# Performance work log

Hardware: AMD Instinct MI355X
Metric: run time of the kernel (lower is better)

Reference implementation:

```python
import jax, jax.numpy as jnp
import numpy as np

H = 128      # hidden_dim
N = 200000   # number of available (job, machine) ops
M = 1000     # machine nodes
J = 5000     # job nodes


def setup_inputs() -> dict:
    key = jax.random.key(0)
    ks = jax.random.split(key, 8)
    s = 0.05  # weight scale
    return {
        "x_graph": jax.random.normal(ks[0], (1, 2 * H), jnp.float32),
        "x_m": jax.random.normal(ks[1], (M, H), jnp.float32),
        "x_job": jax.random.normal(ks[2], (J, H), jnp.float32),
        "m_ids": jax.random.randint(ks[3], (N,), 0, M),
        "job_idx": jax.random.randint(ks[4], (N,), 0, J),
        "W0": jax.random.normal(ks[5], (4 * H, H), jnp.float32) * s,
        "b0": jnp.zeros((H,), jnp.float32),
        "W1": jax.random.normal(ks[6], (H, H), jnp.float32) * s,
        "b1": jnp.zeros((H,), jnp.float32),
        "W2": jax.random.normal(ks[7], (H, 1), jnp.float32) * s,
        "b2": jnp.zeros((1,), jnp.float32),
    }


def reference(x_graph, x_m, x_job, m_ids, job_idx, W0, b0, W1, b1, W2, b2):
    n = m_ids.shape[0]
    # vectorized form of the python loop: [x_graph | x_m[m_id] | x_job[job_pos]] -> [N, 4H]
    feats = jnp.concatenate(
        [
            jnp.broadcast_to(x_graph, (n, x_graph.shape[1])),
            x_m[m_ids],
            x_job[job_idx],
        ],
        axis=1,
    )
    h = jax.nn.relu(feats @ W0 + b0)   # Linear(4H -> H) + ReLU
    h = jax.nn.relu(h @ W1 + b1)       # Linear(H -> H) + ReLU
    scores = (h @ W2 + b2)[:, 0]       # Linear(H -> 1), squeeze -> [N]
    logp = jax.nn.log_softmax(scores, axis=0)
    probs = jnp.exp(logp)
    idx = jnp.argmax(scores)           # greedy selection (deterministic baseline)
    entropy = -jnp.sum(probs * logp)   # Categorical entropy
    return idx, probs[idx], logp[idx], entropy
```

## Files before the change

kernel.cpp:

```cpp
#include <hip/hip_runtime.h>
#include <math.h>

#define HID 128
#define TILE_R 64
#define TILE_P 32
#define XS_STRIDE 132
#define H0S_STRIDE 136
#define DELTA 0.05f
#define MAIN_GRID 1042

typedef short bf16x8 __attribute__((ext_vector_type(8)));
typedef float f32x4 __attribute__((ext_vector_type(4)));

static __device__ __forceinline__ unsigned short f2bf(float f) {
    union { float f; unsigned u; } v; v.f = f;
    unsigned r = v.u + 0x7FFFu + ((v.u >> 16) & 1u);
    return (unsigned short)(r >> 16);
}
static __device__ __forceinline__ float bflo(unsigned u) {
    union { unsigned u; float f; } v; v.u = u << 16; return v.f;
}
static __device__ __forceinline__ float bfhi(unsigned u) {
    union { unsigned u; float f; } v; v.u = u & 0xFFFF0000u; return v.f;
}

#define FMA4(avc, wv)                         \
    acc[r][0] = fmaf(avc, wv.x, acc[r][0]);   \
    acc[r][1] = fmaf(avc, wv.y, acc[r][1]);   \
    acc[r][2] = fmaf(avc, wv.z, acc[r][2]);   \
    acc[r][3] = fmaf(avc, wv.w, acc[r][3]);

__global__ __launch_bounds__(256, 4) void precompute_kernel(
    const float* __restrict__ x_graph,
    const float* __restrict__ x_m,
    const float* __restrict__ x_job,
    const float* __restrict__ W0,
    const float* __restrict__ b0,
    const float* __restrict__ W1,
    float* __restrict__ g,
    unsigned short* __restrict__ Pbf,
    unsigned short* __restrict__ W1T,
    int M, int J, int aTiles, int bTiles)
{
    const int t = threadIdx.x;
    const int bid = blockIdx.x;

    if (bid == 0) {
        __shared__ float xg[2 * HID];
        if (t < HID) { xg[t] = x_graph[t]; xg[t + HID] = x_graph[t + HID]; }
        __syncthreads();
        if (t < HID) {
            float acc = b0[t];
            #pragma unroll 8
            for (int k = 0; k < 2 * HID; ++k)
                acc = fmaf(xg[k], W0[k * HID + t], acc);
            g[t] = acc;
        }
        return;
    }
    if (bid == 1 + aTiles + bTiles) {
        for (int e = t; e < HID * HID; e += 256) {
            int n = e >> 7, k = e & 127;
            W1T[e] = f2bf(W1[k * HID + n]);
        }
        return;
    }

    const int tb = bid - 1;
    const float* X;
    const float* W;
    int r0, nr, dstBase;
    if (tb < aTiles) {
        r0 = tb * TILE_P;
        nr = min(TILE_P, M - r0);
        X = x_m + (size_t)r0 * HID;
        W = W0 + 2 * HID * HID;
        dstBase = r0;
    } else {
        int jb = tb - aTiles;
        r0 = jb * TILE_P;
        nr = min(TILE_P, J - r0);
        X = x_job + (size_t)r0 * HID;
        W = W0 + 3 * HID * HID;
        dstBase = M + r0;
    }

    __shared__ float xs[TILE_P * XS_STRIDE];
    {
        int row = t >> 3;
        int e = t & 7;
        #pragma unroll
        for (int u = 0; u < 4; ++u) {
            int c = e * 16 + u * 4;
            float4 v = (row < nr) ? *(const float4*)(X + row * HID + c)
                                  : make_float4(0.f, 0.f, 0.f, 0.f);
            *(float4*)&xs[row * XS_STRIDE + c] = v;
        }
    }
    __syncthreads();

    const int w = t >> 6;
    const int l = t & 63;
    const int tc = l & 7;
    const int tr = l >> 3;
    const int c0 = w * 32 + tc * 4;

    float acc[4][4];
    #pragma unroll
    for (int r = 0; r < 4; ++r)
        #pragma unroll
        for (int c = 0; c < 4; ++c) acc[r][c] = 0.0f;

    #pragma unroll 2
    for (int k0 = 0; k0 < HID; k0 += 4) {
        float4 w0v = *(const float4*)(W + (k0 + 0) * HID + c0);
        float4 w1v = *(const float4*)(W + (k0 + 1) * HID + c0);
        float4 w2m = *(const float4*)(W + (k0 + 2) * HID + c0);
        float4 w3v = *(const float4*)(W + (k0 + 3) * HID + c0);
        #pragma unroll
        for (int r = 0; r < 4; ++r) {
            float4 a = *(const float4*)&xs[(r * 8 + tr) * XS_STRIDE + k0];
            FMA4(a.x, w0v)
            FMA4(a.y, w1v)
            FMA4(a.z, w2m)
            FMA4(a.w, w3v)
        }
    }

    #pragma unroll
    for (int r = 0; r < 4; ++r) {
        int row = r * 8 + tr;
        if (row < nr) {
            unsigned lo0 = (unsigned)f2bf(acc[r][0]) | ((unsigned)f2bf(acc[r][1]) << 16);
            unsigned lo1 = (unsigned)f2bf(acc[r][2]) | ((unsigned)f2bf(acc[r][3]) << 16);
            uint2 pk = make_uint2(lo0, lo1);
            *(uint2*)(Pbf + (size_t)(dstBase + row) * HID + c0) = pk;
        }
    }
}

__global__ __launch_bounds__(256, 3) void main_kernel(
    const int* __restrict__ m_ids,
    const int* __restrict__ job_idx,
    const float* __restrict__ b1,
    const float* __restrict__ W2,
    const float* __restrict__ b2,
    const float* __restrict__ g,
    const unsigned short* __restrict__ Pbf,
    const unsigned short* __restrict__ W1T,
    float* __restrict__ scores,
    float4* __restrict__ partials,
    float* __restrict__ tmax,
    int N, int M, int tiles)
{
    __shared__ __align__(16) short h0s[TILE_R * H0S_STRIDE];
    __shared__ __align__(16) short w1s[HID * H0S_STRIDE];
    __shared__ float sred[TILE_R];

    const int t = threadIdx.x;
    const int l = t & 63;
    const int w = t >> 6;
    const int quad = l >> 4;
    const int mrow = l & 15;

    {
        const uint4* src = (const uint4*)W1T;
        #pragma unroll
        for (int e = t; e < 2048; e += 256) {
            int n = e >> 4, pos = e & 15;
            *(uint4*)&w1s[n * H0S_STRIDE + pos * 8] = src[e];
        }
    }

    for (int tile = blockIdx.x; tile < tiles; tile += MAIN_GRID) {
        const int row0 = tile * TILE_R;

        {
            int row = t >> 2;
            int q = t & 3;
            int grow = row0 + row;
            int gr = (grow < N) ? grow : (N - 1);
            int m = m_ids[gr];
            int j = job_idx[gr];
            const unsigned short* pm = Pbf + (size_t)m * HID + q * 32;
            const unsigned short* pj = Pbf + (size_t)(M + j) * HID + q * 32;
            const float* gp = g + q * 32;
            short* dst = &h0s[row * H0S_STRIDE + q * 32];
            #pragma unroll
            for (int u = 0; u < 4; ++u) {
                uint4 mv = *(const uint4*)(pm + u * 8);
                uint4 jv = *(const uint4*)(pj + u * 8);
                float4 g0 = *(const float4*)(gp + u * 8);
                float4 g1 = *(const float4*)(gp + u * 8 + 4);
                float h0v = fmaxf(bflo(mv.x) + bflo(jv.x) + g0.x, 0.f);
                float h1v = fmaxf(bfhi(mv.x) + bfhi(jv.x) + g0.y, 0.f);
                float h2v = fmaxf(bflo(mv.y) + bflo(jv.y) + g0.z, 0.f);
                float h3v = fmaxf(bfhi(mv.y) + bfhi(jv.y) + g0.w, 0.f);
                float h4v = fmaxf(bflo(mv.z) + bflo(jv.z) + g1.x, 0.f);
                float h5v = fmaxf(bfhi(mv.z) + bfhi(jv.z) + g1.y, 0.f);
                float h6v = fmaxf(bflo(mv.w) + bflo(jv.w) + g1.z, 0.f);
                float h7v = fmaxf(bfhi(mv.w) + bfhi(jv.w) + g1.w, 0.f);
                uint4 pk;
                pk.x = (unsigned)f2bf(h0v) | ((unsigned)f2bf(h1v) << 16);
                pk.y = (unsigned)f2bf(h2v) | ((unsigned)f2bf(h3v) << 16);
                pk.z = (unsigned)f2bf(h4v) | ((unsigned)f2bf(h5v) << 16);
                pk.w = (unsigned)f2bf(h6v) | ((unsigned)f2bf(h7v) << 16);
                *(uint4*)(dst + u * 8) = pk;
            }
        }
        __syncthreads();

        bf16x8 af[4];
        const short* ab = &h0s[(w * 16 + mrow) * H0S_STRIDE + quad * 8];
        #pragma unroll
        for (int kc = 0; kc < 4; ++kc)
            af[kc] = *(const bf16x8*)(ab + kc * 32);

        f32x4 acc[8];
        #pragma unroll
        for (int nt = 0; nt < 8; ++nt) {
            f32x4 z = {0.f, 0.f, 0.f, 0.f};
            acc[nt] = z;
        }

        const short* bb = &w1s[mrow * H0S_STRIDE + quad * 8];
        #pragma unroll
        for (int nt = 0; nt < 8; ++nt) {
            #pragma unroll
            for (int kc = 0; kc < 4; ++kc) {
                bf16x8 bfr = *(const bf16x8*)(bb + nt * 16 * H0S_STRIDE + kc * 32);
                acc[nt] = __builtin_amdgcn_mfma_f32_16x16x32_bf16(af[kc], bfr, acc[nt], 0, 0, 0);
            }
        }

        float p0 = 0.f, p1 = 0.f, p2 = 0.f, p3 = 0.f;
        #pragma unroll
        for (int nt = 0; nt < 8; ++nt) {
            int c = nt * 16 + mrow;
            float b1v = b1[c], w2v = W2[c];
            p0 += fmaxf(acc[nt][0] + b1v, 0.f) * w2v;
            p1 += fmaxf(acc[nt][1] + b1v, 0.f) * w2v;
            p2 += fmaxf(acc[nt][2] + b1v, 0.f) * w2v;
            p3 += fmaxf(acc[nt][3] + b1v, 0.f) * w2v;
        }
        #pragma unroll
        for (int off = 1; off < 16; off <<= 1) {
            p0 += __shfl_xor(p0, off);
            p1 += __shfl_xor(p1, off);
            p2 += __shfl_xor(p2, off);
            p3 += __shfl_xor(p3, off);
        }
        if (mrow == 0) {
            int rb = w * 16 + quad * 4;
            sred[rb + 0] = p0;
            sred[rb + 1] = p1;
            sred[rb + 2] = p2;
            sred[rb + 3] = p3;
        }
        __syncthreads();

        if (t < 64) {
            int grow = row0 + t;
            float s = sred[t] + b2[0];
            if (grow < N) scores[grow] = s;
            else s = -1e30f;

            float mmax = s;
            int midx = grow;
            #pragma unroll
            for (int off = 1; off < 64; off <<= 1) {
                float om = __shfl_xor(mmax, off);
                int oi = __shfl_xor(midx, off);
                if (om > mmax || (om == mmax && oi < midx)) { mmax = om; midx = oi; }
            }
            float d = s - mmax;
            float e = expf(d);
            float z = e;
            float ss = d * e;
            #pragma unroll
            for (int off = 1; off < 64; off <<= 1) {
                z += __shfl_xor(z, off);
                ss += __shfl_xor(ss, off);
            }
            if (t == 0) {
                partials[tile] = make_float4(mmax, z, ss, (float)midx);
                tmax[tile] = mmax;
            }
        }
    }
}

__device__ inline void sm_merge(float& am, float& az, float& ass, int& ai,
                                float bm, float bz, float bss, int bi)
{
    if (bm > am || (bm == am && bi < ai)) {
        float tm = am, tz = az, ts = ass; int ti = ai;
        am = bm; az = bz; ass = bss; ai = bi;
        bm = tm; bz = tz; bss = ts; bi = ti;
    }
    float f = expf(bm - am);
    az += bz * f;
    ass += (bss + (bm - am) * bz) * f;
}

__global__ __launch_bounds__(256) void scan_kernel(
    const float* __restrict__ tmax, int nparts,
    const float* __restrict__ scores,
    const int* __restrict__ m_ids,
    const int* __restrict__ job_idx,
    const float* __restrict__ x_m,
    const float* __restrict__ x_job,
    const float* __restrict__ W0,
    const float* __restrict__ W1,
    const float* __restrict__ b1,
    const float* __restrict__ W2,
    const float* __restrict__ b2,
    const float* __restrict__ g,
    float2* __restrict__ bests,
    int N)
{
    __shared__ int cand[256];
    __shared__ int ccount;
    __shared__ float rs[4];
    __shared__ int ri[4];
    __shared__ float mmx[4];

    const int t = threadIdx.x;
    const int w = t >> 6;
    const int l = t & 63;
    const int base = blockIdx.x * 256;

    float m0 = -1e30f, m1 = -1e30f, m2 = -1e30f, m3 = -1e30f;
    int i = t;
    for (; i + 768 < nparts; i += 1024) {
        m0 = fmaxf(m0, tmax[i]);
        m1 = fmaxf(m1, tmax[i + 256]);
        m2 = fmaxf(m2, tmax[i + 512]);
        m3 = fmaxf(m3, tmax[i + 768]);
    }
    for (; i < nparts; i += 256) m0 = fmaxf(m0, tmax[i]);
    float mhat = fmaxf(fmaxf(m0, m1), fmaxf(m2, m3));
    #pragma unroll
    for (int off = 1; off < 64; off <<= 1)
        mhat = fmaxf(mhat, __shfl_xor(mhat, off));
    if (l == 0) mmx[w] = mhat;
    if (t == 0) ccount = 0;
    __syncthreads();
    mhat = fmaxf(fmaxf(mmx[0], mmx[1]), fmaxf(mmx[2], mmx[3]));
    const float cut = mhat - DELTA;

    int idx = base + t;
    if (idx < N && scores[idx] >= cut) {
        int p = atomicAdd(&ccount, 1);
        cand[p] = idx;
    }
    __syncthreads();
    const int nc = ccount;
    if (nc == 0) {
        if (t == 0) bests[blockIdx.x] = make_float2(-1e30f, __int_as_float(0x7fffffff));
        return;
    }

    float bs = -1e30f;
    int bi = 0x7fffffff;
    for (int c = w; c < nc; c += 4) {
        int gr = cand[c];
        int mm = m_ids[gr];
        int jj = job_idx[gr];
        const float* xm = x_m + (size_t)mm * HID;
        const float* xj = x_job + (size_t)jj * HID;
        const float* wm = W0 + 2 * HID * HID;
        const float* wj = W0 + 3 * HID * HID;
        float a0 = g[l], a1 = g[l + 64];
        for (int k = 0; k < HID; ++k) {
            float xmk = xm[k];
            float xjk = xj[k];
            a0 = fmaf(xmk, wm[k * HID + l], a0);
            a1 = fmaf(xmk, wm[k * HID + l + 64], a1);
            a0 = fmaf(xjk, wj[k * HID + l], a0);
            a1 = fmaf(xjk, wj[k * HID + l + 64], a1);
        }
        a0 = fmaxf(a0, 0.f);
        a1 = fmaxf(a1, 0.f);
        float acc0 = 0.f, acc1 = 0.f;
        for (int k = 0; k < 64; ++k) {
            float h = __shfl(a0, k);
            acc0 = fmaf(h, W1[k * HID + l], acc0);
            acc1 = fmaf(h, W1[k * HID + l + 64], acc1);
        }
        for (int k = 0; k < 64; ++k) {
            float h = __shfl(a1, k);
            acc0 = fmaf(h, W1[(k + 64) * HID + l], acc0);
            acc1 = fmaf(h, W1[(k + 64) * HID + l + 64], acc1);
        }
        float p = fmaxf(acc0 + b1[l], 0.f) * W2[l]
                + fmaxf(acc1 + b1[l + 64], 0.f) * W2[l + 64];
        #pragma unroll
        for (int off = 1; off < 64; off <<= 1)
            p += __shfl_xor(p, off);
        float s = p + b2[0];
        if (s > bs || (s == bs && gr < bi)) { bs = s; bi = gr; }
    }
    if (l == 0) { rs[w] = bs; ri[w] = bi; }
    __syncthreads();
    if (t == 0) {
        float best = rs[0];
        int bwin = ri[0];
        for (int i2 = 1; i2 < 4; ++i2)
            if (rs[i2] > best || (rs[i2] == best && ri[i2] < bwin)) {
                best = rs[i2]; bwin = ri[i2];
            }
        bests[blockIdx.x] = make_float2(best, __int_as_float(bwin));
    }
}

__global__ __launch_bounds__(256) void finalize_kernel(
    const float4* __restrict__ partials, int nparts,
    const float2* __restrict__ bests, int nblocks,
    float* __restrict__ out)
{
    __shared__ float4 wred[4];
    __shared__ int widx[4];
    __shared__ float rs[4];
    __shared__ int ri[4];
    const int t = threadIdx.x;
    const int w = t >> 6;
    const int l = t & 63;

    float m = -1e30f, z = 0.f, ss = 0.f;
    int idx = 0x7fffffff;
    for (int i = t; i < nparts; i += 256) {
        float4 p = partials[i];
        sm_merge(m, z, ss, idx, p.x, p.y, p.z, (int)p.w);
    }
    #pragma unroll
    for (int off = 1; off < 64; off <<= 1) {
        float om = __shfl_xor(m, off);
        float oz = __shfl_xor(z, off);
        float os = __shfl_xor(ss, off);
        int oi = __shfl_xor(idx, off);
        sm_merge(m, z, ss, idx, om, oz, os, oi);
    }
    if (l == 0) { wred[w] = make_float4(m, z, ss, 0.f); widx[w] = idx; }

    float bs = -1e30f;
    int bi = 0x7fffffff;
    for (int i = t; i < nblocks; i += 256) {
        float2 b = bests[i];
        int gi = __float_as_int(b.y);
        if (b.x > bs || (b.x == bs && gi < bi)) { bs = b.x; bi = gi; }
    }
    #pragma unroll
    for (int off = 1; off < 64; off <<= 1) {
        float os = __shfl_xor(bs, off);
        int oi = __shfl_xor(bi, off);
        if (os > bs || (os == bs && oi < bi)) { bs = os; bi = oi; }
    }
    if (l == 0) { rs[w] = bs; ri[w] = bi; }
    __syncthreads();

    if (t == 0) {
        for (int i = 1; i < 4; ++i) {
            sm_merge(m, z, ss, idx, wred[i].x, wred[i].y, wred[i].z, widx[i]);
            if (rs[i] > bs || (rs[i] == bs && ri[i] < bi)) { bs = rs[i]; bi = ri[i]; }
        }
        float logZ = logf(z);
        out[0] = (float)bi;
        out[1] = expf(bs - m) / z;
        out[2] = (bs - m) - logZ;
        out[3] = logZ - ss / z;
    }
}

extern "C" void kernel_launch(void* const* d_in, const int* in_sizes, int n_in,
                              void* d_out, int out_size, void* d_ws, size_t ws_size,
                              hipStream_t stream)
{
    const float* x_graph = (const float*)d_in[0];
    const float* x_m     = (const float*)d_in[1];
    const float* x_job   = (const float*)d_in[2];
    const int*   m_ids   = (const int*)d_in[3];
    const int*   job_idx = (const int*)d_in[4];
    const float* W0      = (const float*)d_in[5];
    const float* b0      = (const float*)d_in[6];
    const float* W1      = (const float*)d_in[7];
    const float* b1      = (const float*)d_in[8];
    const float* W2      = (const float*)d_in[9];
    const float* b2      = (const float*)d_in[10];
    float* out = (float*)d_out;

    const int N = in_sizes[3];
    const int M = in_sizes[1] / HID;
    const int J = in_sizes[2] / HID;

    const int tiles = (N + TILE_R - 1) / TILE_R;
    const int aTiles = (M + TILE_P - 1) / TILE_P;
    const int bTiles = (J + TILE_P - 1) / TILE_P;
    const int sblocks = (N + 255) / 256;

    float* ws = (float*)d_ws;
    float* g = ws;
    float* scores = ws + HID;
    float4* partials = (float4*)(scores + N);
    float* tmax = (float*)(partials + tiles);
    const int tmaxPad = (tiles + 3) & ~3;
    float2* bests = (float2*)(tmax + tmaxPad);
    unsigned short* W1T = (unsigned short*)(bests + sblocks + (sblocks & 1));
    unsigned short* Pbf = W1T + HID * HID;

    precompute_kernel<<<1 + aTiles + bTiles + 1, 256, 0, stream>>>(
        x_graph, x_m, x_job, W0, b0, W1, g, Pbf, W1T, M, J, aTiles, bTiles);
    main_kernel<<<MAIN_GRID, 256, 0, stream>>>(
        m_ids, job_idx, b1, W2, b2, g, Pbf, W1T, scores, partials, tmax,
        N, M, tiles);
    scan_kernel<<<sblocks, 256, 0, stream>>>(
        tmax, tiles, scores, m_ids, job_idx, x_m, x_job, W0, W1, b1, W2, b2,
        g, bests, N);
    finalize_kernel<<<1, 256, 0, stream>>>(partials, tiles, bests, sblocks, out);
}
```

Measured before the change: 141.1 us.

## Fuse finalize into scan via atomics and last-block reduction, shrink main grid

Each main-kernel tile now publishes its maximum score with a global atomicMax on an order-preserving integer key. Every scan block used to re-reduce the whole per-tile max array; now it reads that single value. The separate finalize kernel is gone. Each scan block atomically max-merges a packed (score, index) key and bumps a completion counter, and the last block merges the softmax partials and writes the outputs. The main grid is also cut from 1042 to 768 blocks. This removes one launch and redundant global reads, at the cost of atomic contention and reliance on counter ordering; the odd increment of 2 on key ties could break the last-block detection.

```diff
diff --git a/kernel.cpp b/kernel.cpp
--- a/kernel.cpp
+++ b/kernel.cpp
@@ -7,7 +7,7 @@
 #define XS_STRIDE 132
 #define H0S_STRIDE 136
 #define DELTA 0.05f
-#define MAIN_GRID 1042
+#define MAIN_GRID 768
 
 typedef short bf16x8 __attribute__((ext_vector_type(8)));
 typedef float f32x4 __attribute__((ext_vector_type(4)));
@@ -22,6 +22,13 @@
 }
 static __device__ __forceinline__ float bfhi(unsigned u) {
     union { unsigned u; float f; } v; v.u = u & 0xFFFF0000u; return v.f;
+}
+static __device__ __forceinline__ unsigned mono32(float f) {
+    unsigned u = __float_as_uint(f);
+    return (u & 0x80000000u) ? ~u : (u | 0x80000000u);
+}
+static __device__ __forceinline__ float unmono32(unsigned k) {
+    return __uint_as_float((k & 0x80000000u) ? (k ^ 0x80000000u) : ~k);
 }
 
 #define FMA4(avc, wv)                         \
@@ -40,12 +47,18 @@
     float* __restrict__ g,
     unsigned short* __restrict__ Pbf,
     unsigned short* __restrict__ W1T,
+    unsigned* __restrict__ misc,
     int M, int J, int aTiles, int bTiles)
 {
     const int t = threadIdx.x;
     const int bid = blockIdx.x;
 
     if (bid == 0) {
+        if (t == 0) {
+            misc[0] = 0u;
+            misc[1] = 0u;
+            *(unsigned long long*)(misc + 2) = 0ull;
+        }
         __shared__ float xg[2 * HID];
         if (t < HID) { xg[t] = x_graph[t]; xg[t + HID] = x_graph[t + HID]; }
         __syncthreads();
@@ -150,7 +163,7 @@
     const unsigned short* __restrict__ W1T,
     float* __restrict__ scores,
     float4* __restrict__ partials,
-    float* __restrict__ tmax,
+    unsigned* __restrict__ misc,
     int N, int M, int tiles)
 {
     __shared__ __align__(16) short h0s[TILE_R * H0S_STRIDE];
@@ -284,7 +297,7 @@
             }
             if (t == 0) {
                 partials[tile] = make_float4(mmax, z, ss, (float)midx);
-                tmax[tile] = mmax;
+                atomicMax(&misc[0], mono32(mmax));
             }
         }
     }
@@ -304,7 +317,7 @@
 }
 
 __global__ __launch_bounds__(256) void scan_kernel(
-    const float* __restrict__ tmax, int nparts,
+    const float4* __restrict__ partials, int nparts,
     const float* __restrict__ scores,
     const int* __restrict__ m_ids,
     const int* __restrict__ job_idx,
@@ -316,38 +329,29 @@
     const float* __restrict__ W2,
     const float* __restrict__ b2,
     const float* __restrict__ g,
-    float2* __restrict__ bests,
+    unsigned* __restrict__ misc,
+    float* __restrict__ out,
     int N)
 {
     __shared__ int cand[256];
     __shared__ int ccount;
     __shared__ float rs[4];
     __shared__ int ri[4];
-    __shared__ float mmx[4];
+    __shared__ int lastFlag;
+    __shared__ float4 wred[4];
+    __shared__ int widx[4];
 
     const int t = threadIdx.x;
     const int w = t >> 6;
     const int l = t & 63;
     const int base = blockIdx.x * 256;
-
-    float m0 = -1e30f, m1 = -1e30f, m2 = -1e30f, m3 = -1e30f;
-    int i = t;
-    for (; i + 768 < nparts; i += 1024) {
-        m0 = fmaxf(m0, tmax[i]);
-        m1 = fmaxf(m1, tmax[i + 256]);
-        m2 = fmaxf(m2, tmax[i + 512]);
-        m3 = fmaxf(m3, tmax[i + 768]);
-    }
-    for (; i < nparts; i += 256) m0 = fmaxf(m0, tmax[i]);
-    float mhat = fmaxf(fmaxf(m0, m1), fmaxf(m2, m3));
-    #pragma unroll
-    for (int off = 1; off < 64; off <<= 1)
-        mhat = fmaxf(mhat, __shfl_xor(mhat, off));
-    if (l == 0) mmx[w] = mhat;
+    unsigned long long* keyp = (unsigned long long*)(misc + 2);
+
     if (t == 0) ccount = 0;
     __syncthreads();
-    mhat = fmaxf(fmaxf(mmx[0], mmx[1]), fmaxf(mmx[2], mmx[3]));
-    const float cut = mhat - DELTA;
+
+    const float mhat_bf = unmono32(misc[0]);
+    const float cut = mhat_bf - DELTA;
 
     int idx = base + t;
     if (idx < N && scores[idx] >= cut) {
@@ -356,10 +360,6 @@
     }
     __syncthreads();
     const int nc = ccount;
-    if (nc == 0) {
-        if (t == 0) bests[blockIdx.x] = make_float2(-1e30f, __int_as_float(0x7fffffff));
-        return;
-    }
 
     float bs = -1e30f;
     int bi = 0x7fffffff;
@@ -403,6 +403,7 @@
     }
     if (l == 0) { rs[w] = bs; ri[w] = bi; }
     __syncthreads();
+
     if (t == 0) {
         float best = rs[0];
         int bwin = ri[0];
@@ -410,65 +411,48 @@
             if (rs[i2] > best || (rs[i2] == best && ri[i2] < bwin)) {
                 best = rs[i2]; bwin = ri[i2];
             }
-        bests[blockIdx.x] = make_float2(best, __int_as_float(bwin));
-    }
-}
-
-__global__ __launch_bounds__(256) void finalize_kernel(
-    const float4* __restrict__ partials, int nparts,
-    const float2* __restrict__ bests, int nblocks,
-    float* __restrict__ out)
-{
-    __shared__ float4 wred[4];
-    __shared__ int widx[4];
-    __shared__ float rs[4];
-    __shared__ int ri[4];
-    const int t = threadIdx.x;
-    const int w = t >> 6;
-    const int l = t & 63;
-
-    float m = -1e30f, z = 0.f, ss = 0.f;
-    int idx = 0x7fffffff;
-    for (int i = t; i < nparts; i += 256) {
-        float4 p = partials[i];
-        sm_merge(m, z, ss, idx, p.x, p.y, p.z, (int)p.w);
-    }
-    #pragma unroll
-    for (int off = 1; off < 64; off <<= 1) {
-        float om = __shfl_xor(m, off);
-        float oz = __shfl_xor(z, off);
-        float os = __shfl_xor(ss, off);
-        int oi = __shfl_xor(idx, off);
-        sm_merge(m, z, ss, idx, om, oz, os, oi);
-    }
-    if (l == 0) { wred[w] = make_float4(m, z, ss, 0.f); widx[w] = idx; }
-
-    float bs = -1e30f;
-    int bi = 0x7fffffff;
-    for (int i = t; i < nblocks; i += 256) {
-        float2 b = bests[i];
-        int gi = __float_as_int(b.y);
-        if (b.x > bs || (b.x == bs && gi < bi)) { bs = b.x; bi = gi; }
-    }
-    #pragma unroll
-    for (int off = 1; off < 64; off <<= 1) {
-        float os = __shfl_xor(bs, off);
-        int oi = __shfl_xor(bi, off);
-        if (os > bs || (os == bs && oi < bi)) { bs = os; bi = oi; }
-    }
-    if (l == 0) { rs[w] = bs; ri[w] = bi; }
+        unsigned inc = 1u;
+        if (nc > 0) {
+            unsigned long long mykey =
+                ((unsigned long long)mono32(best) << 32)
+                | (unsigned long long)(0xFFFFFFFFu - (unsigned)bwin);
+            unsigned long long old = atomicMax(keyp, mykey);
+            inc = (old == mykey) ? 2u : 1u;
+        }
+        unsigned total = atomicAdd(&misc[1], inc) + inc;
+        lastFlag = (total == (unsigned)gridDim.x) ? 1 : 0;
+    }
     __syncthreads();
 
-    if (t == 0) {
-        for (int i = 1; i < 4; ++i) {
-            sm_merge(m, z, ss, idx, wred[i].x, wred[i].y, wred[i].z, widx[i]);
-            if (rs[i] > bs || (rs[i] == bs && ri[i] < bi)) { bs = rs[i]; bi = ri[i]; }
-        }
-        float logZ = logf(z);
-        out[0] = (float)bi;
-        out[1] = expf(bs - m) / z;
-        out[2] = (bs - m) - logZ;
-        out[3] = logZ - ss / z;
+    if (lastFlag) {
+        float m = -1e30f, z = 0.f, ss = 0.f;
+        int midx = 0x7fffffff;
+        for (int i = t; i < nparts; i += 256) {
+            float4 p = partials[i];
+            sm_merge(m, z, ss, midx, p.x, p.y, p.z, (int)p.w);
+        }
+        #pragma unroll
+        for (int off = 1; off < 64; off <<= 1) {
+            float om = __shfl_xor(m, off);
+            float oz = __shfl_xor(z, off);
+            float os = __shfl_xor(ss, off);
+            int oi = __shfl_xor(midx, off);
+            sm_merge(m, z, ss, midx, om, oz, os, oi);
+        }
+        if (l == 0) { wred[w] = make_float4(m, z, ss, 0.f); widx[w] = midx; }
+        __syncthreads();
+        if (t == 0) {
+            for (int i = 1; i < 4; ++i)
+                sm_merge(m, z, ss, midx, wred[i].x, wred[i].y, wred[i].z, widx[i]);
+            unsigned long long key = atomicMax(keyp, 0ull);
+            float swin = unmono32((unsigned)(key >> 32));
+            int iwin = (int)(0xFFFFFFFFu - (unsigned)(key & 0xFFFFFFFFu));
+            float logZ = logf(z);
+            out[0] = (float)iwin;
+            out[1] = expf(swin - m) / z;
+            out[2] = (swin - m) - logZ;
+            out[3] = logZ - ss / z;
+        }
     }
 }
 
@@ -502,19 +486,16 @@
     float* g = ws;
     float* scores = ws + HID;
     float4* partials = (float4*)(scores + N);
-    float* tmax = (float*)(partials + tiles);
-    const int tmaxPad = (tiles + 3) & ~3;
-    float2* bests = (float2*)(tmax + tmaxPad);
-    unsigned short* W1T = (unsigned short*)(bests + sblocks + (sblocks & 1));
+    unsigned* misc = (unsigned*)(partials + tiles);
+    unsigned short* W1T = (unsigned short*)(misc + 4);
     unsigned short* Pbf = W1T + HID * HID;
 
     precompute_kernel<<<1 + aTiles + bTiles + 1, 256, 0, stream>>>(
-        x_graph, x_m, x_job, W0, b0, W1, g, Pbf, W1T, M, J, aTiles, bTiles);
+        x_graph, x_m, x_job, W0, b0, W1, g, Pbf, W1T, misc, M, J, aTiles, bTiles);
     main_kernel<<<MAIN_GRID, 256, 0, stream>>>(
-        m_ids, job_idx, b1, W2, b2, g, Pbf, W1T, scores, partials, tmax,
+        m_ids, job_idx, b1, W2, b2, g, Pbf, W1T, scores, partials, misc,
         N, M, tiles);
     scan_kernel<<<sblocks, 256, 0, stream>>>(
-        tmax, tiles, scores, m_ids, job_idx, x_m, x_job, W0, W1, b1, W2, b2,
-        g, bests, N);
-    finalize_kernel<<<1, 256, 0, stream>>>(partials, tiles, bests, sblocks, out);
-}
+        partials, tiles, scores, m_ids, job_idx, x_m, x_job, W0, W1, b1, W2, b2,
+        g, misc, out, N);
+}
```

Result: slower. 163.2 us (+15.6%).

## Keep W1 fragments in registers and split output columns across waves

Applied to the files above, without the earlier changes.

The persistent grid-stride main kernel becomes a one-block-per-tile launch. W1 is no longer staged in shared memory: each wave loads its 32-column slice of W1 straight into registers as MFMA B fragments. Each wave now covers all 64 rows for its 32 columns, so partial dot-products with W2 are combined across waves through a larger shared reduction array. Shared memory per block drops sharply and launch bounds rise to 4 blocks per CU, at the cost of every block reloading W1 fragments from global memory or cache.

```diff
diff --git a/kernel.cpp b/kernel.cpp
--- a/kernel.cpp
+++ b/kernel.cpp
@@ -7,7 +7,6 @@
 #define XS_STRIDE 132
 #define H0S_STRIDE 136
 #define DELTA 0.05f
-#define MAIN_GRID 1042
 
 typedef short bf16x8 __attribute__((ext_vector_type(8)));
 typedef float f32x4 __attribute__((ext_vector_type(4)));
@@ -139,7 +138,7 @@
     }
 }
 
-__global__ __launch_bounds__(256, 3) void main_kernel(
+__global__ __launch_bounds__(256, 4) void main_kernel(
     const int* __restrict__ m_ids,
     const int* __restrict__ job_idx,
     const float* __restrict__ b1,
@@ -151,141 +150,135 @@
     float* __restrict__ scores,
     float4* __restrict__ partials,
     float* __restrict__ tmax,
-    int N, int M, int tiles)
+    int N, int M)
 {
     __shared__ __align__(16) short h0s[TILE_R * H0S_STRIDE];
-    __shared__ __align__(16) short w1s[HID * H0S_STRIDE];
-    __shared__ float sred[TILE_R];
+    __shared__ float sred[4 * TILE_R];
 
     const int t = threadIdx.x;
     const int l = t & 63;
     const int w = t >> 6;
     const int quad = l >> 4;
     const int mrow = l & 15;
-
+    const int row0 = blockIdx.x * TILE_R;
+
+    bf16x8 bfr[2][4];
     {
-        const uint4* src = (const uint4*)W1T;
-        #pragma unroll
-        for (int e = t; e < 2048; e += 256) {
-            int n = e >> 4, pos = e & 15;
-            *(uint4*)&w1s[n * H0S_STRIDE + pos * 8] = src[e];
-        }
-    }
-
-    for (int tile = blockIdx.x; tile < tiles; tile += MAIN_GRID) {
-        const int row0 = tile * TILE_R;
-
-        {
-            int row = t >> 2;
-            int q = t & 3;
-            int grow = row0 + row;
-            int gr = (grow < N) ? grow : (N - 1);
-            int m = m_ids[gr];
-            int j = job_idx[gr];
-            const unsigned short* pm = Pbf + (size_t)m * HID + q * 32;
-            const unsigned short* pj = Pbf + (size_t)(M + j) * HID + q * 32;
-            const float* gp = g + q * 32;
-            short* dst = &h0s[row * H0S_STRIDE + q * 32];
+        const unsigned short* wb = W1T + (size_t)(w * 32 + mrow) * HID + quad * 8;
+        #pragma unroll
+        for (int nt = 0; nt < 2; ++nt)
             #pragma unroll
-            for (int u = 0; u < 4; ++u) {
-                uint4 mv = *(const uint4*)(pm + u * 8);
-                uint4 jv = *(const uint4*)(pj + u * 8);
-                float4 g0 = *(const float4*)(gp + u * 8);
-                float4 g1 = *(const float4*)(gp + u * 8 + 4);
-                float h0v = fmaxf(bflo(mv.x) + bflo(jv.x) + g0.x, 0.f);
-                float h1v = fmaxf(bfhi(mv.x) + bfhi(jv.x) + g0.y, 0.f);
-                float h2v = fmaxf(bflo(mv.y) + bflo(jv.y) + g0.z, 0.f);
-                float h3v = fmaxf(bfhi(mv.y) + bfhi(jv.y) + g0.w, 0.f);
-                float h4v = fmaxf(bflo(mv.z) + bflo(jv.z) + g1.x, 0.f);
-                float h5v = fmaxf(bfhi(mv.z) + bfhi(jv.z) + g1.y, 0.f);
-                float h6v = fmaxf(bflo(mv.w) + bflo(jv.w) + g1.z, 0.f);
-                float h7v = fmaxf(bfhi(mv.w) + bfhi(jv.w) + g1.w, 0.f);
-                uint4 pk;
-                pk.x = (unsigned)f2bf(h0v) | ((unsigned)f2bf(h1v) << 16);
-                pk.y = (unsigned)f2bf(h2v) | ((unsigned)f2bf(h3v) << 16);
-                pk.z = (unsigned)f2bf(h4v) | ((unsigned)f2bf(h5v) << 16);
-                pk.w = (unsigned)f2bf(h6v) | ((unsigned)f2bf(h7v) << 16);
-                *(uint4*)(dst + u * 8) = pk;
-            }
-        }
-        __syncthreads();
-
-        bf16x8 af[4];
-        const short* ab = &h0s[(w * 16 + mrow) * H0S_STRIDE + quad * 8];
-        #pragma unroll
-        for (int kc = 0; kc < 4; ++kc)
-            af[kc] = *(const bf16x8*)(ab + kc * 32);
-
-        f32x4 acc[8];
-        #pragma unroll
-        for (int nt = 0; nt < 8; ++nt) {
-            f32x4 z = {0.f, 0.f, 0.f, 0.f};
-            acc[nt] = z;
-        }
-
-        const short* bb = &w1s[mrow * H0S_STRIDE + quad * 8];
-        #pragma unroll
-        for (int nt = 0; nt < 8; ++nt) {
+            for (int kc = 0; kc < 4; ++kc)
+                bfr[nt][kc] = *(const bf16x8*)(wb + nt * 16 * HID + kc * 32);
+    }
+    const float b1v0 = b1[w * 32 + mrow];
+    const float b1v1 = b1[w * 32 + 16 + mrow];
+    const float w2v0 = W2[w * 32 + mrow];
+    const float w2v1 = W2[w * 32 + 16 + mrow];
+
+    {
+        int row = t >> 2;
+        int q = t & 3;
+        int grow = row0 + row;
+        int gr = (grow < N) ? grow : (N - 1);
+        int m = m_ids[gr];
+        int j = job_idx[gr];
+        const unsigned short* pm = Pbf + (size_t)m * HID + q * 32;
+        const unsigned short* pj = Pbf + (size_t)(M + j) * HID + q * 32;
+        const float* gp = g + q * 32;
+        short* dst = &h0s[row * H0S_STRIDE + q * 32];
+        #pragma unroll
+        for (int u = 0; u < 4; ++u) {
+            uint4 mv = *(const uint4*)(pm + u * 8);
+            uint4 jv = *(const uint4*)(pj + u * 8);
+            float4 g0 = *(const float4*)(gp + u * 8);
+            float4 g1 = *(const float4*)(gp + u * 8 + 4);
+            float h0v = fmaxf(bflo(mv.x) + bflo(jv.x) + g0.x, 0.f);
+            float h1v = fmaxf(bfhi(mv.x) + bfhi(jv.x) + g0.y, 0.f);
+            float h2v = fmaxf(bflo(mv.y) + bflo(jv.y) + g0.z, 0.f);
+            float h3v = fmaxf(bfhi(mv.y) + bfhi(jv.y) + g0.w, 0.f);
+            float h4v = fmaxf(bflo(mv.z) + bflo(jv.z) + g1.x, 0.f);
+            float h5v = fmaxf(bfhi(mv.z) + bfhi(jv.z) + g1.y, 0.f);
+            float h6v = fmaxf(bflo(mv.w) + bflo(jv.w) + g1.z, 0.f);
+            float h7v = fmaxf(bfhi(mv.w) + bfhi(jv.w) + g1.w, 0.f);
+            uint4 pk;
+            pk.x = (unsigned)f2bf(h0v) | ((unsigned)f2bf(h1v) << 16);
+            pk.y = (unsigned)f2bf(h2v) | ((unsigned)f2bf(h3v) << 16);
+            pk.z = (unsigned)f2bf(h4v) | ((unsigned)f2bf(h5v) << 16);
+            pk.w = (unsigned)f2bf(h6v) | ((unsigned)f2bf(h7v) << 16);
+            *(uint4*)(dst + u * 8) = pk;
+        }
+    }
+    __syncthreads();
+
+    f32x4 acc[4][2];
+    #pragma unroll
+    for (int mt = 0; mt < 4; ++mt) {
+        f32x4 z = {0.f, 0.f, 0.f, 0.f};
+        acc[mt][0] = z;
+        acc[mt][1] = z;
+    }
+    #pragma unroll
+    for (int mt = 0; mt < 4; ++mt) {
+        const short* ab = &h0s[(mt * 16 + mrow) * H0S_STRIDE + quad * 8];
+        #pragma unroll
+        for (int kc = 0; kc < 4; ++kc) {
+            bf16x8 af = *(const bf16x8*)(ab + kc * 32);
+            acc[mt][0] = __builtin_amdgcn_mfma_f32_16x16x32_bf16(af, bfr[0][kc], acc[mt][0], 0, 0, 0);
+            acc[mt][1] = __builtin_amdgcn_mfma_f32_16x16x32_bf16(af, bfr[1][kc], acc[mt][1], 0, 0, 0);
+        }
+    }
+
+    #pragma unroll
+    for (int mt = 0; mt < 4; ++mt) {
+        float p[4];
+        #pragma unroll
+        for (int i = 0; i < 4; ++i) {
+            p[i] = fmaxf(acc[mt][0][i] + b1v0, 0.f) * w2v0
+                 + fmaxf(acc[mt][1][i] + b1v1, 0.f) * w2v1;
+        }
+        #pragma unroll
+        for (int off = 1; off < 16; off <<= 1) {
             #pragma unroll
-            for (int kc = 0; kc < 4; ++kc) {
-                bf16x8 bfr = *(const bf16x8*)(bb + nt * 16 * H0S_STRIDE + kc * 32);
-                acc[nt] = __builtin_amdgcn_mfma_f32_16x16x32_bf16(af[kc], bfr, acc[nt], 0, 0, 0);
-            }
-        }
-
-        float p0 = 0.f, p1 = 0.f, p2 = 0.f, p3 = 0.f;
-        #pragma unroll
-        for (int nt = 0; nt < 8; ++nt) {
-            int c = nt * 16 + mrow;
-            float b1v = b1[c], w2v = W2[c];
-            p0 += fmaxf(acc[nt][0] + b1v, 0.f) * w2v;
-            p1 += fmaxf(acc[nt][1] + b1v, 0.f) * w2v;
-            p2 += fmaxf(acc[nt][2] + b1v, 0.f) * w2v;
-            p3 += fmaxf(acc[nt][3] + b1v, 0.f) * w2v;
-        }
-        #pragma unroll
-        for (int off = 1; off < 16; off <<= 1) {
-            p0 += __shfl_xor(p0, off);
-            p1 += __shfl_xor(p1, off);
-            p2 += __shfl_xor(p2, off);
-            p3 += __shfl_xor(p3, off);
+            for (int i = 0; i < 4; ++i)
+                p[i] += __shfl_xor(p[i], off);
         }
         if (mrow == 0) {
-            int rb = w * 16 + quad * 4;
-            sred[rb + 0] = p0;
-            sred[rb + 1] = p1;
-            sred[rb + 2] = p2;
-            sred[rb + 3] = p3;
-        }
-        __syncthreads();
-
-        if (t < 64) {
-            int grow = row0 + t;
-            float s = sred[t] + b2[0];
-            if (grow < N) scores[grow] = s;
-            else s = -1e30f;
-
-            float mmax = s;
-            int midx = grow;
-            #pragma unroll
-            for (int off = 1; off < 64; off <<= 1) {
-                float om = __shfl_xor(mmax, off);
-                int oi = __shfl_xor(midx, off);
-                if (om > mmax || (om == mmax && oi < midx)) { mmax = om; midx = oi; }
-            }
-            float d = s - mmax;
-            float e = expf(d);
-            float z = e;
-            float ss = d * e;
-            #pragma unroll
-            for (int off = 1; off < 64; off <<= 1) {
-                z += __shfl_xor(z, off);
-                ss += __shfl_xor(ss, off);
-            }
-            if (t == 0) {
-                partials[tile] = make_float4(mmax, z, ss, (float)midx);
-                tmax[tile] = mmax;
-            }
+            int rb = mt * 16 + quad * 4;
+            sred[w * TILE_R + rb + 0] = p[0];
+            sred[w * TILE_R + rb + 1] = p[1];
+            sred[w * TILE_R + rb + 2] = p[2];
+            sred[w * TILE_R + rb + 3] = p[3];
+        }
+    }
+    __syncthreads();
+
+    if (t < 64) {
+        int grow = row0 + t;
+        float s = sred[t] + sred[64 + t] + sred[128 + t] + sred[192 + t] + b2[0];
+        if (grow < N) scores[grow] = s;
+        else s = -1e30f;
+
+        float mmax = s;
+        int midx = grow;
+        #pragma unroll
+        for (int off = 1; off < 64; off <<= 1) {
+            float om = __shfl_xor(mmax, off);
+            int oi = __shfl_xor(midx, off);
+            if (om > mmax || (om == mmax && oi < midx)) { mmax = om; midx = oi; }
+        }
+        float d = s - mmax;
+        float e = expf(d);
+        float z = e;
+        float ss = d * e;
+        #pragma unroll
+        for (int off = 1; off < 64; off <<= 1) {
+            z += __shfl_xor(z, off);
+            ss += __shfl_xor(ss, off);
+        }
+        if (t == 0) {
+            partials[blockIdx.x] = make_float4(mmax, z, ss, (float)midx);
+            tmax[blockIdx.x] = mmax;
         }
     }
 }
@@ -510,9 +503,8 @@
 
     precompute_kernel<<<1 + aTiles + bTiles + 1, 256, 0, stream>>>(
         x_graph, x_m, x_job, W0, b0, W1, g, Pbf, W1T, M, J, aTiles, bTiles);
-    main_kernel<<<MAIN_GRID, 256, 0, stream>>>(
-        m_ids, job_idx, b1, W2, b2, g, Pbf, W1T, scores, partials, tmax,
-        N, M, tiles);
+    main_kernel<<<tiles, 256, 0, stream>>>(
+        m_ids, job_idx, b1, W2, b2, g, Pbf, W1T, scores, partials, tmax, N, M);
     scan_kernel<<<sblocks, 256, 0, stream>>>(
         tmax, tiles, scores, m_ids, job_idx, x_m, x_job, W0, W1, b1, W2, b2,
         g, bests, N);
```

Result: slower. 147.2 us (+4.3%).
